# Optimization experiments

Hardware: AMD Instinct MI355X
Metric: run time of the kernel (lower is better)

## Reference

```python
import jax, jax.numpy as jnp
import numpy as np

LN_EPS = 1e-5


def _layernorm(x, g, b):
    m = jnp.mean(x, axis=-1, keepdims=True)
    v = jnp.mean((x - m) ** 2, axis=-1, keepdims=True)
    return (x - m) * jax.lax.rsqrt(v + LN_EPS) * g + b


def _gcn_conv(x, row, col, ew, W, b):
    # linear projection
    x = x @ W + b  # [N, out]
    n = x.shape[0]
    # weighted degree per source node (index_add over row)
    deg = jax.ops.segment_sum(ew, row, num_segments=n)  # [N]
    safe = jnp.where(deg > 0, deg, 1.0)
    dis = jnp.where(deg > 0, jax.lax.rsqrt(safe), 0.0)  # deg^-0.5, inf -> 0
    norm = dis[row] * ew * dis[col]  # [E]
    # gather-scale-scatter aggregation
    return jax.ops.segment_sum(norm[:, None] * x[col], row, num_segments=n)


def setup_inputs() -> dict:
    key = jax.random.key(0)
    ks = jax.random.split(key, 8)
    N, E, D_IN, D_H, D_OUT = 50000, 800000, 384, 256, 128
    x = jax.random.normal(ks[0], (N, D_IN), dtype=jnp.float32)
    edge_index = jax.random.randint(ks[1], (2, E), 0, N, dtype=jnp.int64)
    edge_weight = jax.random.uniform(ks[2], (E,), dtype=jnp.float32)
    W1 = jax.random.normal(ks[3], (D_IN, D_H), dtype=jnp.float32) * 0.02
    b1 = jnp.zeros((D_H,), dtype=jnp.float32)
    W2 = jax.random.normal(ks[4], (D_H, D_OUT), dtype=jnp.float32) * 0.02
    b2 = jnp.zeros((D_OUT,), dtype=jnp.float32)
    g1 = jnp.ones((D_H,), dtype=jnp.float32)
    be1 = jnp.zeros((D_H,), dtype=jnp.float32)
    g2 = jnp.ones((D_OUT,), dtype=jnp.float32)
    be2 = jnp.zeros((D_OUT,), dtype=jnp.float32)
    return {"x": x, "edge_index": edge_index, "edge_weight": edge_weight,
            "W1": W1, "b1": b1, "W2": W2, "b2": b2,
            "g1": g1, "be1": be1, "g2": g2, "be2": be2}


def reference(x, edge_index, edge_weight, W1, b1, W2, b2, g1, be1, g2, be2):
    row, col = edge_index[0], edge_index[1]
    h = _gcn_conv(x, row, col, edge_weight, W1, b1)
    h = _layernorm(h, g1, be1)
    h = jax.nn.relu(h)
    # dropout is identity in eval mode
    h = _gcn_conv(h, row, col, edge_weight, W2, b2)
    h = _layernorm(h, g2, be2)
    return h
```

## Files before the change

kernel.cpp:

```cpp
#include <hip/hip_runtime.h>


constexpr float LN_EPS = 1e-5f;

typedef __attribute__((ext_vector_type(8))) short short8;
typedef __attribute__((ext_vector_type(4))) float f32x4;

static __device__ __forceinline__ unsigned short f2bf(float f) {
    unsigned u = __float_as_uint(f);
    u += 0x7FFFu + ((u >> 16) & 1u);
    return (unsigned short)(u >> 16);
}
static __device__ __forceinline__ float bf2f(unsigned short h) {
    return __uint_as_float(((unsigned)h) << 16);
}
static __device__ __forceinline__ short8 f2bf8(float4 a, float4 b) {
    short8 r;
    r[0] = (short)f2bf(a.x); r[1] = (short)f2bf(a.y);
    r[2] = (short)f2bf(a.z); r[3] = (short)f2bf(a.w);
    r[4] = (short)f2bf(b.x); r[5] = (short)f2bf(b.y);
    r[6] = (short)f2bf(b.z); r[7] = (short)f2bf(b.w);
    return r;
}

#if defined(__has_builtin)
#if __has_builtin(__builtin_amdgcn_global_load_lds)
#define HAS_GLL 1
#endif
#endif

#ifdef HAS_GLL
static __device__ __forceinline__ void gll16(const void* g, void* l) {
    __builtin_amdgcn_global_load_lds(
        (__attribute__((address_space(1))) void*)g,
        (__attribute__((address_space(3))) void*)l, 16, 0, 0);
}
#endif

static __device__ __forceinline__ int swz(int r) {
    return (r & 3) ^ ((r >> 2) & 3);
}

__global__ __launch_bounds__(256) void k_hist(
    const int* __restrict__ row, const float* __restrict__ ew,
    unsigned long long* __restrict__ packed, int* __restrict__ ord, int E)
{
    int e = blockIdx.x * 256 + threadIdx.x;
    if (e >= E) return;
    int r = row[e];
    unsigned fx = __float2uint_rn(ew[e] * 16777216.0f);
    unsigned long long old =
        atomicAdd(packed + r, (1ULL << 32) | (unsigned long long)fx);
    ord[e] = (int)(old >> 32);
}

__global__ __launch_bounds__(256) void k_dis_part(
    const unsigned long long* __restrict__ packed, float* __restrict__ dis,
    int* __restrict__ part, int n)
{
    int i = blockIdx.x * 256 + threadIdx.x;
    int v = 0;
    if (i < n) {
        unsigned long long p = packed[i];
        float d = (float)(unsigned)(p & 0xFFFFFFFFu) * (1.0f / 16777216.0f);
        dis[i] = d > 0.0f ? rsqrtf(d) : 0.0f;
        v = (int)(p >> 32);
    }
    #pragma unroll
    for (int off = 32; off; off >>= 1) v += __shfl_xor(v, off);
    __shared__ int ws[4];
    if ((threadIdx.x & 63) == 0) ws[threadIdx.x >> 6] = v;
    __syncthreads();
    if (threadIdx.x == 0) part[blockIdx.x] = ws[0] + ws[1] + ws[2] + ws[3];
}

__global__ __launch_bounds__(256) void k_scanpart(int* part, int nparts)
{
    int t = threadIdx.x;
    int v = (t < nparts) ? part[t] : 0;
    __shared__ int s[256];
    s[t] = v; __syncthreads();
    for (int off = 1; off < 256; off <<= 1) {
        int u = (t >= off) ? s[t - off] : 0;
        __syncthreads();
        s[t] += u;
        __syncthreads();
    }
    if (t < nparts) part[t] = s[t] - v;
}

__global__ __launch_bounds__(256) void k_rowptr(
    const unsigned long long* __restrict__ packed, const int* __restrict__ part,
    int* __restrict__ rowptr, int n)
{
    int t = threadIdx.x;
    int i = blockIdx.x * 256 + t;
    int v = (i < n) ? (int)(packed[i] >> 32) : 0;
    __shared__ int s[256];
    s[t] = v; __syncthreads();
    for (int off = 1; off < 256; off <<= 1) {
        int u = (t >= off) ? s[t - off] : 0;
        __syncthreads();
        s[t] += u;
        __syncthreads();
    }
    if (i < n) {
        int base = part[blockIdx.x];
        rowptr[i] = base + s[t] - v;
        if (i == n - 1) rowptr[n] = base + s[t];
    }
}

__global__ __launch_bounds__(256) void k_scatter(
    const int* __restrict__ row, const int* __restrict__ col,
    const float* __restrict__ ew, const float* __restrict__ dis,
    const int* __restrict__ rowptr, const int* __restrict__ ord,
    int2* __restrict__ edges, int E)
{
    int e = blockIdx.x * 256 + threadIdx.x;
    if (e >= E) return;
    int r = row[e], c = col[e];
    int p = rowptr[r] + ord[e];
    edges[p] = make_int2(c, __float_as_int(dis[r] * ew[e] * dis[c]));
}

__global__ __launch_bounds__(256) void k_xbf(
    const float* __restrict__ x, unsigned short* __restrict__ xb, int nwin)
{
    int w = blockIdx.x * 256 + threadIdx.x;
    if (w >= nwin) return;
    int row = w / 12, win = w - row * 12;
    int s = swz(row & 15);
    const float* src = x + (size_t)row * 384 + win * 32;
    unsigned short* dst = xb + (size_t)row * 384 + win * 32;
    #pragma unroll
    for (int c = 0; c < 4; ++c) {
        int cs = c ^ s;
        float4 a = *(const float4*)(src + cs * 8);
        float4 b = *(const float4*)(src + cs * 8 + 4);
        *(short8*)(dst + c * 8) = f2bf8(a, b);
    }
}

__global__ __launch_bounds__(256) void k_wt(
    const float* __restrict__ W1, const float* __restrict__ W2,
    unsigned short* __restrict__ W1P, unsigned short* __restrict__ W2P)
{
    constexpr int K1 = 384, N1 = 256, K2 = 256, N2 = 128;
    int o = blockIdx.x * 256 + threadIdx.x;
    if (o < K1 * N1) {
        int cc = o & 31, n = (o >> 5) % N1, p = o / (N1 * 32);
        int c = cc >> 3, j = cc & 7;
        int k = p * 32 + (((c ^ swz(n & 15)) & 3) << 3) + j;
        W1P[o] = f2bf(W1[(size_t)k * N1 + n]);
    } else {
        int o2 = o - K1 * N1;
        if (o2 < K2 * N2) {
            int cc = o2 & 31, n = (o2 >> 5) % N2, p = o2 / (N2 * 32);
            int c = cc >> 3, j = cc & 7;
            int k = p * 32 + (((c ^ swz(n & 15)) & 3) << 3) + j;
            W2P[o2] = f2bf(W2[(size_t)k * N2 + n]);
        }
    }
}

template<int NFULL, int K>
__global__ __launch_bounds__(256, 4) void k_gemm_mfma(
    const unsigned short* __restrict__ A, const unsigned short* __restrict__ BP,
    const float* __restrict__ bias, unsigned short* __restrict__ C, int M)
{
    constexpr int BM = 64, BN = 128, BK = 32;
    constexpr int MR = 4, NF = 2;
    constexpr int AB = BM * BK * 2;
    constexpr int BB = BN * BK * 2;
    constexpr int TB = AB + BB;

    __shared__ char smem[2 * TB];

    const int t    = threadIdx.x;
    const int lane = t & 63;
    const int wid  = t >> 6;
    const int row0 = blockIdx.x * BM;
    const int col0 = blockIdx.y * BN;
    const int fr   = lane & 15;
    const int fq   = lane >> 4;
    const int nbw  = wid * 32;
    const int nt   = K / BK;

    const int cOff = ((fq ^ swz(fr)) & 3) << 3;

    f32x4 acc[MR][NF] = {};

    auto srcA = [&](int slot, int k0) -> const void* {
        int ra = slot >> 2, ca = slot & 3;
        int gr = row0 + ra; if (gr >= M) gr = M - 1;
        return (const void*)(A + (size_t)gr * K + k0 + ca * 8);
    };
    auto srcB = [&](int slot, int st) -> const void* {
        int rb = slot >> 2, cb = slot & 3;
        return (const void*)(BP + ((size_t)st * NFULL + col0 + rb) * 32 + cb * 8);
    };

    auto compute = [&](char* buf) {
        const unsigned short* As = (const unsigned short*)buf;
        const unsigned short* Bs = (const unsigned short*)(buf + AB);
        short8 af[MR], bfr[NF];
        #pragma unroll
        for (int i = 0; i < MR; ++i)
            af[i] = *(const short8*)(As + (i * 16 + fr) * 32 + cOff);
        #pragma unroll
        for (int j = 0; j < NF; ++j)
            bfr[j] = *(const short8*)(Bs + (nbw + j * 16 + fr) * 32 + cOff);
        #pragma unroll
        for (int i = 0; i < MR; ++i)
            #pragma unroll
            for (int j = 0; j < NF; ++j)
                acc[i][j] = __builtin_amdgcn_mfma_f32_16x16x32_bf16(
                    af[i], bfr[j], acc[i][j], 0, 0, 0);
    };

#ifdef HAS_GLL
    auto stage = [&](int buf, int st) {
        char* As = smem + buf * TB;
        char* Bs = As + AB;
        gll16(srcA(t, st * BK), As + t * 16);
        gll16(srcB(t, st), Bs + t * 16);
        gll16(srcB(256 + t, st), Bs + (256 + t) * 16);
    };

    stage(0, 0);
    __syncthreads();
    int cur = 0;
    for (int st = 0; st < nt; ++st) {
        if (st + 1 < nt) stage(cur ^ 1, st + 1);
        compute(smem + cur * TB);
        __syncthreads();
        cur ^= 1;
    }
#else
    for (int st = 0; st < nt; ++st) {
        int4 ar = *(const int4*)srcA(t, st * BK);
        int4 b0 = *(const int4*)srcB(t, st);
        int4 b1 = *(const int4*)srcB(256 + t, st);
        __syncthreads();
        *(int4*)(smem + t * 16) = ar;
        *(int4*)(smem + AB + t * 16) = b0;
        *(int4*)(smem + AB + (256 + t) * 16) = b1;
        __syncthreads();
        compute(smem);
    }
#endif

    #pragma unroll
    for (int i = 0; i < MR; ++i) {
        #pragma unroll
        for (int j = 0; j < NF; ++j) {
            const int c = col0 + nbw + j * 16 + fr;
            const float bvv = bias[c];
            #pragma unroll
            for (int r = 0; r < 4; ++r) {
                const int rr = row0 + i * 16 + fq * 4 + r;
                if (rr < M)
                    C[(size_t)rr * NFULL + c] = f2bf(acc[i][j][r] + bvv);
            }
        }
    }
}

template<int D, bool RELU, bool OUTBF, bool SWZ>
__global__ __launch_bounds__(256) void k_agg_ln(
    const unsigned short* __restrict__ feat, const int* __restrict__ rowptr,
    const int2* __restrict__ edges,
    const float* __restrict__ g, const float* __restrict__ b,
    void* __restrict__ outv, int n)
{
    constexpr int LPR = D / 8;
    constexpr int EPI = 64 / LPR;
    const int gw   = (blockIdx.x * 256 + threadIdx.x) >> 6;
    const int lane = threadIdx.x & 63;
    if (gw >= n) return;

    const int sub = lane / LPR;
    const int el  = (lane % LPR) * 8;

    float acc[8] = {};
    const int j0 = rowptr[gw], j1 = rowptr[gw + 1];
    #pragma unroll 2
    for (int j = j0; j < j1; j += EPI) {
        const int jj = j + sub;
        float wv = 0.0f;
        int   c  = 0;
        if (jj < j1) {
            int2 e = edges[jj];
            c  = e.x;
            wv = __int_as_float(e.y);
        }
        const short8 u = *(const short8*)(feat + (size_t)c * D + el);
        #pragma unroll
        for (int i = 0; i < 8; ++i)
            acc[i] += wv * bf2f((unsigned short)u[i]);
    }

    #pragma unroll
    for (int off = LPR; off < 64; off <<= 1)
        #pragma unroll
        for (int i = 0; i < 8; ++i)
            acc[i] += __shfl_xor(acc[i], off);

    float s = 0.0f;
    #pragma unroll
    for (int i = 0; i < 8; ++i) s += acc[i];
    #pragma unroll
    for (int off = 32; off; off >>= 1) s += __shfl_xor(s, off);
    const float m = s * (1.0f / (EPI * D));

    float q = 0.0f;
    #pragma unroll
    for (int i = 0; i < 8; ++i) { float d = acc[i] - m; q += d * d; }
    #pragma unroll
    for (int off = 32; off; off >>= 1) q += __shfl_xor(q, off);
    const float r = rsqrtf(q * (1.0f / (EPI * D)) + LN_EPS);

    if (lane < LPR) {
        float4 g0 = *(const float4*)(g + el);
        float4 g1 = *(const float4*)(g + el + 4);
        float4 b0 = *(const float4*)(b + el);
        float4 b1 = *(const float4*)(b + el + 4);
        float gg[8] = {g0.x, g0.y, g0.z, g0.w, g1.x, g1.y, g1.z, g1.w};
        float bb[8] = {b0.x, b0.y, b0.z, b0.w, b1.x, b1.y, b1.z, b1.w};
        float o[8];
        #pragma unroll
        for (int i = 0; i < 8; ++i) {
            float tv = (acc[i] - m) * r * gg[i] + bb[i];
            if constexpr (RELU) tv = fmaxf(tv, 0.0f);
            o[i] = tv;
        }
        if constexpr (OUTBF) {
            int eo = el;
            if constexpr (SWZ) {
                int sA = swz(gw & 15);
                eo = (el & ~31) | ((((el >> 3) & 3) ^ sA) << 3);
            }
            short8 u;
            #pragma unroll
            for (int i = 0; i < 8; ++i) u[i] = (short)f2bf(o[i]);
            *(short8*)((unsigned short*)outv + (size_t)gw * D + eo) = u;
        } else {
            float* op = (float*)outv + (size_t)gw * D + el;
            *(float4*)(op)     = make_float4(o[0], o[1], o[2], o[3]);
            *(float4*)(op + 4) = make_float4(o[4], o[5], o[6], o[7]);
        }
    }
}

extern "C" void kernel_launch(void* const* d_in, const int* in_sizes, int n_in,
                              void* d_out, int out_size, void* d_ws, size_t ws_size,
                              hipStream_t stream)
{
    (void)n_in; (void)out_size; (void)ws_size;

    constexpr int DIN = 384, DH = 256, DOUT = 128;

    const float* x   = (const float*)d_in[0];
    const int*   ei  = (const int*)  d_in[1];
    const float* ew  = (const float*)d_in[2];
    const float* W1  = (const float*)d_in[3];
    const float* b1  = (const float*)d_in[4];
    const float* W2  = (const float*)d_in[5];
    const float* b2  = (const float*)d_in[6];
    const float* g1  = (const float*)d_in[7];
    const float* be1 = (const float*)d_in[8];
    const float* g2  = (const float*)d_in[9];
    const float* be2 = (const float*)d_in[10];
    float* out = (float*)d_out;

    const int N = in_sizes[0] / DIN;
    const int E = in_sizes[2];
    const int* row = ei;
    const int* col = ei + E;

    char* w = (char*)d_ws;
    auto carve = [&](size_t bytes) {
        char* p = w;
        w += (bytes + 255) & ~(size_t)255;
        return p;
    };
    unsigned long long* packed = (unsigned long long*)carve((size_t)N * 8);
    float*          dis    = (float*)carve((size_t)N * 4);
    int*            rowptr = (int*)  carve((size_t)(N + 1) * 4);
    int*            part   = (int*)  carve(256 * 4);
    int2*           edges  = (int2*) carve((size_t)E * 8);
    unsigned short* W1P    = (unsigned short*)carve((size_t)DIN * DH * 2);
    unsigned short* W2P    = (unsigned short*)carve((size_t)DH * DOUT * 2);
    unsigned short* x_bf   = (unsigned short*)carve((size_t)N * DIN * 2);
    unsigned short* h1     = (unsigned short*)carve((size_t)N * DH * 2);
    unsigned short* h1ln   = (unsigned short*)carve((size_t)N * DH * 2);
    unsigned short* h2     = (unsigned short*)carve((size_t)N * DOUT * 2);
    int*            ord    = (int*)h1;

    const int gE = (E + 255) / 256;
    const int gN = (N + 255) / 256;
    const int gW = (N + 3) / 4;
    const int gG = (N + 63) / 64;
    const int gX = (N * 12 + 255) / 256;

    hipMemsetAsync(packed, 0, (size_t)N * 8, stream);
    k_hist    <<<gE, 256, 0, stream>>>(row, ew, packed, ord, E);
    k_dis_part<<<gN, 256, 0, stream>>>(packed, dis, part, N);
    k_scanpart<<<1, 256, 0, stream>>>(part, gN);
    k_rowptr  <<<gN, 256, 0, stream>>>(packed, part, rowptr, N);
    k_scatter <<<gE, 256, 0, stream>>>(row, col, ew, dis, rowptr, ord, edges, E);

    k_wt <<<(DIN * DH + DH * DOUT + 255) / 256, 256, 0, stream>>>(W1, W2, W1P, W2P);
    k_xbf<<<gX, 256, 0, stream>>>(x, x_bf, N * 12);

    {
        dim3 grid(gG, DH / 128);
        k_gemm_mfma<DH, DIN><<<grid, 256, 0, stream>>>(x_bf, W1P, b1, h1, N);
    }
    k_agg_ln<DH, true, true, true><<<gW, 256, 0, stream>>>(h1, rowptr, edges,
                                                           g1, be1, h1ln, N);

    {
        dim3 grid(gG, DOUT / 128);
        k_gemm_mfma<DOUT, DH><<<grid, 256, 0, stream>>>(h1ln, W2P, b2, h2, N);
    }
    k_agg_ln<DOUT, false, false, false><<<gW, 256, 0, stream>>>(h2, rowptr, edges,
                                                                g2, be2, out, N);
}
```

Baseline: 234.4 us.

## Prefetch edges in aggregation, widen per-lane features, and merge small prep kernels

The aggregation kernel now handles 16 features per lane instead of 8 and software-pipelines edge and feature loads two iterations ahead to hide gather latency. It unpacks bf16 pairs into packed float2 FMAs. The partial-sum scan is folded into the rowptr kernel, with each block redoing the small scan, and the weight and x conversions are merged into one launch. Together these cut launch count and are meant to raise memory-level parallelism in the gather, at the cost of more registers and redundant scan work per block.

```diff
diff --git a/kernel.cpp b/kernel.cpp
--- a/kernel.cpp
+++ b/kernel.cpp
@@ -5,14 +5,12 @@
 
 typedef __attribute__((ext_vector_type(8))) short short8;
 typedef __attribute__((ext_vector_type(4))) float f32x4;
+typedef __attribute__((ext_vector_type(2))) float f32x2;
 
 static __device__ __forceinline__ unsigned short f2bf(float f) {
     unsigned u = __float_as_uint(f);
     u += 0x7FFFu + ((u >> 16) & 1u);
     return (unsigned short)(u >> 16);
-}
-static __device__ __forceinline__ float bf2f(unsigned short h) {
-    return __uint_as_float(((unsigned)h) << 16);
 }
 static __device__ __forceinline__ short8 f2bf8(float4 a, float4 b) {
     short8 r;
@@ -74,11 +72,26 @@
     if (threadIdx.x == 0) part[blockIdx.x] = ws[0] + ws[1] + ws[2] + ws[3];
 }
 
-__global__ __launch_bounds__(256) void k_scanpart(int* part, int nparts)
+__global__ __launch_bounds__(256) void k_rowptr(
+    const unsigned long long* __restrict__ packed, const int* __restrict__ part,
+    int* __restrict__ rowptr, int n, int nparts)
 {
     int t = threadIdx.x;
-    int v = (t < nparts) ? part[t] : 0;
     __shared__ int s[256];
+
+    int pv = (t < nparts) ? part[t] : 0;
+    s[t] = pv; __syncthreads();
+    for (int off = 1; off < 256; off <<= 1) {
+        int u = (t >= off) ? s[t - off] : 0;
+        __syncthreads();
+        s[t] += u;
+        __syncthreads();
+    }
+    const int base = (blockIdx.x == 0) ? 0 : s[blockIdx.x - 1];
+    __syncthreads();
+
+    int i = blockIdx.x * 256 + t;
+    int v = (i < n) ? (int)(packed[i] >> 32) : 0;
     s[t] = v; __syncthreads();
     for (int off = 1; off < 256; off <<= 1) {
         int u = (t >= off) ? s[t - off] : 0;
@@ -86,26 +99,7 @@
         s[t] += u;
         __syncthreads();
     }
-    if (t < nparts) part[t] = s[t] - v;
-}
-
-__global__ __launch_bounds__(256) void k_rowptr(
-    const unsigned long long* __restrict__ packed, const int* __restrict__ part,
-    int* __restrict__ rowptr, int n)
-{
-    int t = threadIdx.x;
-    int i = blockIdx.x * 256 + t;
-    int v = (i < n) ? (int)(packed[i] >> 32) : 0;
-    __shared__ int s[256];
-    s[t] = v; __syncthreads();
-    for (int off = 1; off < 256; off <<= 1) {
-        int u = (t >= off) ? s[t - off] : 0;
-        __syncthreads();
-        s[t] += u;
-        __syncthreads();
-    }
     if (i < n) {
-        int base = part[blockIdx.x];
         rowptr[i] = base + s[t] - v;
         if (i == n - 1) rowptr[n] = base + s[t];
     }
@@ -124,42 +118,41 @@
     edges[p] = make_int2(c, __float_as_int(dis[r] * ew[e] * dis[c]));
 }
 
-__global__ __launch_bounds__(256) void k_xbf(
-    const float* __restrict__ x, unsigned short* __restrict__ xb, int nwin)
-{
-    int w = blockIdx.x * 256 + threadIdx.x;
-    if (w >= nwin) return;
-    int row = w / 12, win = w - row * 12;
-    int s = swz(row & 15);
-    const float* src = x + (size_t)row * 384 + win * 32;
-    unsigned short* dst = xb + (size_t)row * 384 + win * 32;
-    #pragma unroll
-    for (int c = 0; c < 4; ++c) {
-        int cs = c ^ s;
-        float4 a = *(const float4*)(src + cs * 8);
-        float4 b = *(const float4*)(src + cs * 8 + 4);
-        *(short8*)(dst + c * 8) = f2bf8(a, b);
-    }
-}
-
-__global__ __launch_bounds__(256) void k_wt(
+__global__ __launch_bounds__(256) void k_prep(
     const float* __restrict__ W1, const float* __restrict__ W2,
-    unsigned short* __restrict__ W1P, unsigned short* __restrict__ W2P)
+    const float* __restrict__ x,
+    unsigned short* __restrict__ W1P, unsigned short* __restrict__ W2P,
+    unsigned short* __restrict__ xb, int nwin)
 {
     constexpr int K1 = 384, N1 = 256, K2 = 256, N2 = 128;
-    int o = blockIdx.x * 256 + threadIdx.x;
-    if (o < K1 * N1) {
-        int cc = o & 31, n = (o >> 5) % N1, p = o / (N1 * 32);
-        int c = cc >> 3, j = cc & 7;
-        int k = p * 32 + (((c ^ swz(n & 15)) & 3) << 3) + j;
-        W1P[o] = f2bf(W1[(size_t)k * N1 + n]);
-    } else {
-        int o2 = o - K1 * N1;
-        if (o2 < K2 * N2) {
+    constexpr int WTB = (K1 * N1 + K2 * N2) / 256;
+    if (blockIdx.x < WTB) {
+        int o = blockIdx.x * 256 + threadIdx.x;
+        if (o < K1 * N1) {
+            int cc = o & 31, n = (o >> 5) % N1, p = o / (N1 * 32);
+            int c = cc >> 3, j = cc & 7;
+            int k = p * 32 + (((c ^ swz(n & 15)) & 3) << 3) + j;
+            W1P[o] = f2bf(W1[(size_t)k * N1 + n]);
+        } else {
+            int o2 = o - K1 * N1;
             int cc = o2 & 31, n = (o2 >> 5) % N2, p = o2 / (N2 * 32);
             int c = cc >> 3, j = cc & 7;
             int k = p * 32 + (((c ^ swz(n & 15)) & 3) << 3) + j;
             W2P[o2] = f2bf(W2[(size_t)k * N2 + n]);
+        }
+    } else {
+        int w = (blockIdx.x - WTB) * 256 + threadIdx.x;
+        if (w >= nwin) return;
+        int row = w / 12, win = w - row * 12;
+        int s = swz(row & 15);
+        const float* src = x + (size_t)row * 384 + win * 32;
+        unsigned short* dst = xb + (size_t)row * 384 + win * 32;
+        #pragma unroll
+        for (int c = 0; c < 4; ++c) {
+            int cs = c ^ s;
+            float4 a = *(const float4*)(src + cs * 8);
+            float4 b = *(const float4*)(src + cs * 8 + 4);
+            *(short8*)(dst + c * 8) = f2bf8(a, b);
         }
     }
 }
@@ -274,81 +267,109 @@
     const float* __restrict__ g, const float* __restrict__ b,
     void* __restrict__ outv, int n)
 {
-    constexpr int LPR = D / 8;
+    constexpr int EV  = 16;
+    constexpr int LPR = D / EV;
     constexpr int EPI = 64 / LPR;
     const int gw   = (blockIdx.x * 256 + threadIdx.x) >> 6;
     const int lane = threadIdx.x & 63;
     if (gw >= n) return;
 
     const int sub = lane / LPR;
-    const int el  = (lane % LPR) * 8;
-
-    float acc[8] = {};
+    const int el  = (lane % LPR) * EV;
+
     const int j0 = rowptr[gw], j1 = rowptr[gw + 1];
-    #pragma unroll 2
+
+    f32x2 acc[8] = {};
+
+    int2 e0 = (j0 + sub < j1)       ? edges[j0 + sub]       : make_int2(0, 0);
+    int2 e1 = (j0 + EPI + sub < j1) ? edges[j0 + EPI + sub] : make_int2(0, 0);
+    uint4 u0, u1;
+    {
+        const unsigned short* p = feat + (size_t)e0.x * D + el;
+        u0 = *(const uint4*)p;
+        u1 = *(const uint4*)(p + 8);
+    }
+
     for (int j = j0; j < j1; j += EPI) {
-        const int jj = j + sub;
-        float wv = 0.0f;
-        int   c  = 0;
-        if (jj < j1) {
-            int2 e = edges[jj];
-            c  = e.x;
-            wv = __int_as_float(e.y);
-        }
-        const short8 u = *(const short8*)(feat + (size_t)c * D + el);
-        #pragma unroll
-        for (int i = 0; i < 8; ++i)
-            acc[i] += wv * bf2f((unsigned short)u[i]);
+        int2 e2 = (j + 2 * EPI + sub < j1) ? edges[j + 2 * EPI + sub]
+                                           : make_int2(0, 0);
+        const unsigned short* p = feat + (size_t)e1.x * D + el;
+        uint4 v0 = *(const uint4*)p;
+        uint4 v1 = *(const uint4*)(p + 8);
+
+        const float wv = __int_as_float(e0.y);
+        const unsigned a[8] = {u0.x, u0.y, u0.z, u0.w, u1.x, u1.y, u1.z, u1.w};
+        #pragma unroll
+        for (int i = 0; i < 8; ++i) {
+            f32x2 h;
+            h.x = __uint_as_float(a[i] << 16);
+            h.y = __uint_as_float(a[i] & 0xffff0000u);
+            acc[i] += h * wv;
+        }
+        u0 = v0; u1 = v1; e0 = e1; e1 = e2;
     }
 
     #pragma unroll
     for (int off = LPR; off < 64; off <<= 1)
         #pragma unroll
-        for (int i = 0; i < 8; ++i)
-            acc[i] += __shfl_xor(acc[i], off);
+        for (int i = 0; i < 8; ++i) {
+            acc[i].x += __shfl_xor(acc[i].x, off);
+            acc[i].y += __shfl_xor(acc[i].y, off);
+        }
 
     float s = 0.0f;
     #pragma unroll
-    for (int i = 0; i < 8; ++i) s += acc[i];
+    for (int i = 0; i < 8; ++i) s += acc[i].x + acc[i].y;
     #pragma unroll
     for (int off = 32; off; off >>= 1) s += __shfl_xor(s, off);
     const float m = s * (1.0f / (EPI * D));
 
     float q = 0.0f;
     #pragma unroll
-    for (int i = 0; i < 8; ++i) { float d = acc[i] - m; q += d * d; }
+    for (int i = 0; i < 8; ++i) {
+        float dx = acc[i].x - m, dy = acc[i].y - m;
+        q += dx * dx + dy * dy;
+    }
     #pragma unroll
     for (int off = 32; off; off >>= 1) q += __shfl_xor(q, off);
     const float r = rsqrtf(q * (1.0f / (EPI * D)) + LN_EPS);
 
     if (lane < LPR) {
-        float4 g0 = *(const float4*)(g + el);
-        float4 g1 = *(const float4*)(g + el + 4);
-        float4 b0 = *(const float4*)(b + el);
-        float4 b1 = *(const float4*)(b + el + 4);
-        float gg[8] = {g0.x, g0.y, g0.z, g0.w, g1.x, g1.y, g1.z, g1.w};
-        float bb[8] = {b0.x, b0.y, b0.z, b0.w, b1.x, b1.y, b1.z, b1.w};
-        float o[8];
-        #pragma unroll
-        for (int i = 0; i < 8; ++i) {
-            float tv = (acc[i] - m) * r * gg[i] + bb[i];
-            if constexpr (RELU) tv = fmaxf(tv, 0.0f);
-            o[i] = tv;
+        float o[16];
+        #pragma unroll
+        for (int i = 0; i < 4; ++i) {
+            float4 gv = *(const float4*)(g + el + i * 4);
+            float4 bv = *(const float4*)(b + el + i * 4);
+            const float vals[4] = {acc[2 * i].x, acc[2 * i].y,
+                                   acc[2 * i + 1].x, acc[2 * i + 1].y};
+            const float gg[4] = {gv.x, gv.y, gv.z, gv.w};
+            const float bb[4] = {bv.x, bv.y, bv.z, bv.w};
+            #pragma unroll
+            for (int k2 = 0; k2 < 4; ++k2) {
+                float tv = (vals[k2] - m) * r * gg[k2] + bb[k2];
+                if constexpr (RELU) tv = fmaxf(tv, 0.0f);
+                o[i * 4 + k2] = tv;
+            }
         }
         if constexpr (OUTBF) {
-            int eo = el;
-            if constexpr (SWZ) {
-                int sA = swz(gw & 15);
-                eo = (el & ~31) | ((((el >> 3) & 3) ^ sA) << 3);
+            short8 lo, hi;
+            #pragma unroll
+            for (int i = 0; i < 8; ++i) {
+                lo[i] = (short)f2bf(o[i]);
+                hi[i] = (short)f2bf(o[8 + i]);
             }
-            short8 u;
-            #pragma unroll
-            for (int i = 0; i < 8; ++i) u[i] = (short)f2bf(o[i]);
-            *(short8*)((unsigned short*)outv + (size_t)gw * D + eo) = u;
+            unsigned short* ob = (unsigned short*)outv + (size_t)gw * D;
+            const int w0 = el & ~31;
+            const int c0 = (el >> 3) & 3;
+            const int sA = SWZ ? swz(gw & 15) : 0;
+            *(short8*)(ob + w0 + (((c0 ^ sA) & 3) << 3))       = lo;
+            *(short8*)(ob + w0 + ((((c0 + 1) ^ sA) & 3) << 3)) = hi;
         } else {
             float* op = (float*)outv + (size_t)gw * D + el;
-            *(float4*)(op)     = make_float4(o[0], o[1], o[2], o[3]);
-            *(float4*)(op + 4) = make_float4(o[4], o[5], o[6], o[7]);
+            *(float4*)(op)      = make_float4(o[0],  o[1],  o[2],  o[3]);
+            *(float4*)(op + 4)  = make_float4(o[4],  o[5],  o[6],  o[7]);
+            *(float4*)(op + 8)  = make_float4(o[8],  o[9],  o[10], o[11]);
+            *(float4*)(op + 12) = make_float4(o[12], o[13], o[14], o[15]);
         }
     }
 }
@@ -403,16 +424,15 @@
     const int gW = (N + 3) / 4;
     const int gG = (N + 63) / 64;
     const int gX = (N * 12 + 255) / 256;
+    constexpr int WTB = (DIN * DH + DH * DOUT) / 256;
 
     hipMemsetAsync(packed, 0, (size_t)N * 8, stream);
     k_hist    <<<gE, 256, 0, stream>>>(row, ew, packed, ord, E);
     k_dis_part<<<gN, 256, 0, stream>>>(packed, dis, part, N);
-    k_scanpart<<<1, 256, 0, stream>>>(part, gN);
-    k_rowptr  <<<gN, 256, 0, stream>>>(packed, part, rowptr, N);
+    k_rowptr  <<<gN, 256, 0, stream>>>(packed, part, rowptr, N, gN);
     k_scatter <<<gE, 256, 0, stream>>>(row, col, ew, dis, rowptr, ord, edges, E);
 
-    k_wt <<<(DIN * DH + DH * DOUT + 255) / 256, 256, 0, stream>>>(W1, W2, W1P, W2P);
-    k_xbf<<<gX, 256, 0, stream>>>(x, x_bf, N * 12);
+    k_prep<<<WTB + gX, 256, 0, stream>>>(W1, W2, x, W1P, W2P, x_bf, N * 12);
 
     {
         dim3 grid(gG, DH / 128);
```

Result: no change. 229.9 us (-2.0%).
